# Performance work log

Hardware: AMD Instinct MI355X
Metric: run time of the kernel (lower is better)

The kernel has to match this reference:

```python
import math
import jax, jax.numpy as jnp
import numpy as np

EPS = 1e-5

def lstm(x, Wih, Whh, b):
    # x: [N,T,D]; PyTorch gate order i,f,g,o; b = b_ih + b_hh combined
    N = x.shape[0]
    H = Whh.shape[1]
    gx = jnp.einsum('ntd,gd->ntg', x, Wih) + b  # [N,T,4H]
    def step(carry, g):
        h, c = carry
        z = g + h @ Whh.T
        i, f, gg, o = jnp.split(z, 4, axis=-1)
        c = jax.nn.sigmoid(f) * c + jax.nn.sigmoid(i) * jnp.tanh(gg)
        h = jax.nn.sigmoid(o) * jnp.tanh(c)
        return (h, c), h
    init = (jnp.zeros((N, H), x.dtype), jnp.zeros((N, H), x.dtype))
    (hN, _), ys = jax.lax.scan(step, init, jnp.swapaxes(gx, 0, 1))
    return jnp.swapaxes(ys, 0, 1), hN  # outputs [N,T,H], h_n [N,H]

def bilstm_layer(x, fW, fU, fb, bW, bU, bb):
    of, _ = lstm(x, fW, fU, fb)
    ob, _ = lstm(x[:, ::-1], bW, bU, bb)
    return jnp.concatenate([of, ob[:, ::-1]], axis=-1)

def layernorm(x, g, b):
    m = jnp.mean(x, -1, keepdims=True)
    v = jnp.mean((x - m) ** 2, -1, keepdims=True)
    return (x - m) * jax.lax.rsqrt(v + EPS) * g + b

def encoder_layer(src, Wq, bq, Wk, bk, Wv, bv, Wo, bo, W1, b1, W2, b2, lng, lnb):
    B, S, d = src.shape
    G, NH = 5, 5
    dk = d // NH
    # group channel shuffle (as in source)
    qs = src.reshape(B, S, G, d // G).swapaxes(-1, -2).reshape(B, S, d)
    q = qs @ Wq.T + bq
    k = q @ Wk.T + bk   # NOTE: source applies W_k/W_v to the projected query
    v = q @ Wv.T + bv
    def heads(t):
        return t.reshape(B, S, NH, dk).transpose(0, 2, 1, 3)
    qh, kh, vh = heads(q), heads(k), heads(v)
    attn = jax.nn.softmax(jnp.einsum('bhqd,bhkd->bhqk', qh, kh) / math.sqrt(dk), axis=-1)
    o = jnp.einsum('bhqk,bhkd->bhqd', attn, vh).transpose(0, 2, 1, 3).reshape(B, S, d)
    o = o @ Wo.T + bo
    src = layernorm(src + o, lng, lnb)          # dropout is identity in eval
    ff = jax.nn.relu(src @ W1.T + b1) @ W2.T + b2
    src = layernorm(src + ff, lng, lnb)         # same LayerNorm params reused
    return src, attn

def _forward(x, qWih, qWhh, qb, kWih, kWhh, kb, vWih, vWhh, vb,
             tWq, tbq, tWk, tbk, tWv, tbv, tWo, tbo, tW1, tb1, tW2, tb2, tlng, tlnb,
             l0fWih, l0fWhh, l0fb, l0bWih, l0bWhh, l0bb,
             l1fWih, l1fWhh, l1fb, l1bWih, l1bWhh, l1bb,
             fc1W, fc1b, fc2W, fc2b):
    B, T, F = x.shape
    H = qWhh.shape[1]
    # per-feature LSTMs: shared weights across features -> batch them
    xf = x.transpose(0, 2, 1).reshape(B * F, T, 1)
    _, hq = lstm(xf, qWih, qWhh, qb)   # [B*F,H]
    _, hk = lstm(xf, kWih, kWhh, kb)   # [B*F,H]
    _, hv = lstm(xf, vWih, vWhh, vb)   # [B*F,1]
    Q = hq.reshape(B, F, H)
    K = hk.reshape(B, F, H)
    V = hv.reshape(B, F)
    # b_ij = (q_i . k_j)/sqrt(H) * v_j, softmax over j
    scores = jnp.einsum('bih,bjh->bij', Q, K) / math.sqrt(H) * V[:, None, :]
    Wsm = jax.nn.softmax(scores, axis=-1)          # [B,F,F] rows indexed by i
    attn_output = jnp.einsum('btj,bij->bti', x, Wsm)  # bmm(x, softmax_b_i)
    b = Wsm.transpose(0, 2, 1)                     # stack(b_list, dim=-1)
    src = jnp.concatenate([x, attn_output], axis=-1)  # [B,T,2F]
    attns = []
    for l in range(2):
        src, a = encoder_layer(src, tWq[l], tbq[l], tWk[l], tbk[l], tWv[l], tbv[l],
                               tWo[l], tbo[l], tW1[l], tb1[l], tW2[l], tb2[l],
                               tlng[l], tlnb[l])
        attns.append(a)
    c = jnp.stack(attns)                           # [2,B,5,T,T]
    out = bilstm_layer(src, l0fWih, l0fWhh, l0fb, l0bWih, l0bWhh, l0bb)
    out = bilstm_layer(out, l1fWih, l1fWhh, l1fb, l1bWih, l1bWhh, l1bb)
    out = jax.nn.relu(out[:, -1, :])               # [B,2H]
    out = jax.nn.relu(out @ fc1W.T + fc1b)
    out = out @ fc2W.T + fc2b                      # [B,1]
    return out, b, c

def setup_inputs() -> dict:
    B, T, F, H = 16, 128, 40, 64
    d = 2 * F
    key = jax.random.key(0)
    ks = iter(jax.random.split(key, 64))
    def n(shape, fan):
        return (jax.random.normal(next(ks), shape) / math.sqrt(fan)).astype(jnp.float32)
    inp = {'x': jax.random.normal(next(ks), (B, T, F), dtype=jnp.float32)}
    # per-feature LSTMs
    inp.update(qWih=n((4 * H, 1), 1), qWhh=n((4 * H, H), H), qb=n((4 * H,), H))
    inp.update(kWih=n((4 * H, 1), 1), kWhh=n((4 * H, H), H), kb=n((4 * H,), H))
    inp.update(vWih=n((4, 1), 1), vWhh=n((4, 1), 1), vb=n((4,), 1))
    # transformer (2 layers stacked on leading axis)
    inp.update(tWq=n((2, d, d), d), tbq=n((2, d), d), tWk=n((2, d, d), d), tbk=n((2, d), d),
               tWv=n((2, d, d), d), tbv=n((2, d), d), tWo=n((2, d, d), d), tbo=n((2, d), d),
               tW1=n((2, 4 * d, d), d), tb1=n((2, 4 * d), d), tW2=n((2, d, 4 * d), 4 * d),
               tb2=n((2, d), 4 * d), tlng=jnp.ones((2, d), jnp.float32), tlnb=jnp.zeros((2, d), jnp.float32))
    # main bidirectional 2-layer LSTM
    inp.update(l0fWih=n((4 * H, d), d), l0fWhh=n((4 * H, H), H), l0fb=n((4 * H,), H),
               l0bWih=n((4 * H, d), d), l0bWhh=n((4 * H, H), H), l0bb=n((4 * H,), H),
               l1fWih=n((4 * H, 2 * H), 2 * H), l1fWhh=n((4 * H, H), H), l1fb=n((4 * H,), H),
               l1bWih=n((4 * H, 2 * H), 2 * H), l1bWhh=n((4 * H, H), H), l1bb=n((4 * H,), H))
    inp.update(fc1W=n((H, 2 * H), 2 * H), fc1b=n((H,), 2 * H), fc2W=n((1, H), H), fc2b=n((1,), H))
    return inp

def reference(x, qWih, qWhh, qb, kWih, kWhh, kb, vWih, vWhh, vb,
              tWq, tbq, tWk, tbk, tWv, tbv, tWo, tbo, tW1, tb1, tW2, tb2, tlng, tlnb,
              l0fWih, l0fWhh, l0fb, l0bWih, l0bWhh, l0bb,
              l1fWih, l1fWhh, l1fb, l1bWih, l1bWhh, l1bb,
              fc1W, fc1b, fc2W, fc2b):
    return _forward(x, qWih, qWhh, qb, kWih, kWhh, kb, vWih, vWhh, vb,
                    tWq, tbq, tWk, tbk, tWv, tbv, tWo, tbo, tW1, tb1, tW2, tb2, tlng, tlnb,
                    l0fWih, l0fWhh, l0fb, l0bWih, l0bWhh, l0bb,
                    l1fWih, l1fWhh, l1fb, l1bWih, l1bWhh, l1bb,
                    fc1W, fc1b, fc2W, fc2b)
```

## Files before the change

kernel.cpp:

```cpp
#include <hip/hip_runtime.h>

__device__ __forceinline__ float sigf(float x){ return 1.0f/(1.0f+__expf(-x)); }
__device__ __forceinline__ float tanhfast(float x){ return 1.0f - 2.0f/(__expf(2.0f*x)+1.0f); }

#define Bn 16
#define Tn 128
#define Fn 40
#define Hn 64
#define Dn 80
#define NHn 5
#define DKn 16
#define FFn 320

#define LD4(p,i) (((const float4*)(p))[i])

#define DECL8(v, p) \
  float4 v##0=LD4(p,0), v##1=LD4(p,1), v##2=LD4(p,2), v##3=LD4(p,3), \
         v##4=LD4(p,4), v##5=LD4(p,5), v##6=LD4(p,6), v##7=LD4(p,7);
#define PIN4(P) asm volatile("" : "+v"(P.x), "+v"(P.y), "+v"(P.z), "+v"(P.w));
#define PIN8(v) PIN4(v##0) PIN4(v##1) PIN4(v##2) PIN4(v##3) PIN4(v##4) PIN4(v##5) \
  PIN4(v##6) PIN4(v##7)

#define ACC8(base) \
  { const float4 h0=hb4[(base)+0]; a += h0.x*w0.x + h0.y*w0.y + h0.z*w0.z + h0.w*w0.w; } \
  { const float4 h1=hb4[(base)+1]; a += h1.x*w1.x + h1.y*w1.y + h1.z*w1.z + h1.w*w1.w; } \
  { const float4 h2=hb4[(base)+2]; a += h2.x*w2.x + h2.y*w2.y + h2.z*w2.z + h2.w*w2.w; } \
  { const float4 h3=hb4[(base)+3]; a += h3.x*w3.x + h3.y*w3.y + h3.z*w3.z + h3.w*w3.w; } \
  { const float4 h4=hb4[(base)+4]; a += h4.x*w4.x + h4.y*w4.y + h4.z*w4.z + h4.w*w4.w; } \
  { const float4 h5=hb4[(base)+5]; a += h5.x*w5.x + h5.y*w5.y + h5.z*w5.z + h5.w*w5.w; } \
  { const float4 h6=hb4[(base)+6]; a += h6.x*w6.x + h6.y*w6.y + h6.z*w6.z + h6.w*w6.w; } \
  { const float4 h7=hb4[(base)+7]; a += h7.x*w7.x + h7.y*w7.y + h7.z*w7.z + h7.w*w7.w; }

__global__ __launch_bounds__(512)
void k_feat_lstm5(
    const float* __restrict__ x,
    const float* __restrict__ qWih, const float* __restrict__ qWhh, const float* __restrict__ qb,
    const float* __restrict__ kWih, const float* __restrict__ kWhh, const float* __restrict__ kb,
    const float* __restrict__ vWih, const float* __restrict__ vWhh, const float* __restrict__ vb,
    float* __restrict__ hq, float* __restrict__ hk, float* __restrict__ hv)
{
  const int blk = blockIdx.x;
  const int t = threadIdx.x;
  if (blk >= 1280){
    const int inst = (blk - 1280)*512 + t;
    if (inst < 640){
      const int bi = inst/Fn, f = inst%Fn;
      const float* xp = x + bi*Tn*Fn + f;
      const float wih0=vWih[0], wih1=vWih[1], wih2=vWih[2], wih3=vWih[3];
      const float u0v=vWhh[0], u1v=vWhh[1], u2v=vWhh[2], u3v=vWhh[3];
      const float c0=vb[0], c1=vb[1], c2=vb[2], c3=vb[3];
      float h=0.f, c=0.f;
      #pragma unroll 1
      for (int tt=0;tt<Tn;++tt){
        float xt = xp[tt*Fn];
        float zi = xt*wih0 + h*u0v + c0;
        float zf = xt*wih1 + h*u1v + c1;
        float zg = xt*wih2 + h*u2v + c2;
        float zo = xt*wih3 + h*u3v + c3;
        c = sigf(zf)*c + sigf(zi)*tanhfast(zg);
        h = sigf(zo)*tanhfast(c);
      }
      hv[inst] = h;
    }
    return;
  }
  const bool isk = blk >= 640;
  const int inst = isk ? blk-640 : blk;
  const int bi = inst/Fn, f = inst%Fn;
  const float* Whh = isk ? kWhh : qWhh;
  const float* Wih = isk ? kWih : qWih;
  const float* bia = isk ? kb  : qb;
  float* outp = isk ? hk : hq;

  const int half = t >> 8;
  const int r    = t & 255;

  DECL8(w, Whh + r*Hn + half*32);
  PIN8(w);
  const float wih = Wih[r];
  const float bb  = bia[r];

  __shared__ __align__(16) float hb[Hn];
  __shared__ float pa[512];
  __shared__ float xls[Tn];

  const float* xp = x + bi*Tn*Fn + f;
  if (t < Tn) xls[t] = xp[t*Fn];
  if (t < Hn) hb[t] = 0.f;
  float c = 0.f, h = 0.f;
  __syncthreads();

  const float4* hb4 = (const float4*)hb;
  const int jbase = half*8;
  #pragma unroll 1
  for (int tt=0;tt<Tn;++tt){
    float a = half ? 0.f : (bb + xls[tt]*wih);
    ACC8(jbase)
    pa[t] = a;
    __syncthreads();
    if (t < Hn){
      const float zi = pa[t    ] + pa[t+256];
      const float zf = pa[t+ 64] + pa[t+320];
      const float zg = pa[t+128] + pa[t+384];
      const float zo = pa[t+192] + pa[t+448];
      c = sigf(zf)*c + sigf(zi)*tanhfast(zg);
      h = sigf(zo)*tanhfast(c);
      hb[t] = h;
    }
    __syncthreads();
  }
  if (t < Hn) outp[inst*Hn + t] = h;
}

__global__ __launch_bounds__(64) void k_featattn(
    const float* __restrict__ hq, const float* __restrict__ hk, const float* __restrict__ hv,
    float* __restrict__ Wsm, float* __restrict__ out_b)
{
  const int blk = blockIdx.x;
  const int bi = blk / Fn, i = blk % Fn;
  const int j = threadIdx.x;
  __shared__ float qrow[Hn];
  qrow[j] = hq[blk*Hn + j];
  __syncthreads();
  float s = -1e30f;
  if (j < Fn){
    const float* krow = hk + (bi*Fn + j)*Hn;
    float a = 0.f;
    #pragma unroll
    for (int h2=0; h2<Hn; ++h2) a += qrow[h2]*krow[h2];
    s = a * 0.125f * hv[bi*Fn + j];
  }
  float m = s;
  #pragma unroll
  for (int off=32; off>0; off>>=1) m = fmaxf(m, __shfl_xor(m, off));
  float e = (j < Fn) ? __expf(s - m) : 0.f;
  float tot = e;
  #pragma unroll
  for (int off=32; off>0; off>>=1) tot += __shfl_xor(tot, off);
  float p = e / tot;
  if (j < Fn){
    Wsm[blk*Fn + j] = p;
    out_b[bi*(Fn*Fn) + j*Fn + i] = p;
  }
}

__global__ __launch_bounds__(128) void k_build_src(
    const float* __restrict__ x, const float* __restrict__ Wsm, float* __restrict__ src)
{
  const int blk = blockIdx.x;
  const int bi = blk / Tn;
  const int tid = threadIdx.x;
  __shared__ float xrow[Fn];
  if (tid < Fn) xrow[tid] = x[blk*Fn + tid];
  __syncthreads();
  if (tid < Fn){
    src[blk*Dn + tid] = xrow[tid];
  } else if (tid < Dn){
    const int i = tid - Fn;
    const float* wrow = Wsm + (bi*Fn + i)*Fn;
    float a = 0.f;
    #pragma unroll
    for (int j2=0;j2<Fn;++j2) a += xrow[j2]*wrow[j2];
    src[blk*Dn + tid] = a;
  }
}

__global__ __launch_bounds__(128) void k_qkv(
    const float* __restrict__ src,
    const float* __restrict__ Wq, const float* __restrict__ bq,
    const float* __restrict__ Wk, const float* __restrict__ bk,
    const float* __restrict__ Wv, const float* __restrict__ bv,
    float* __restrict__ q, float* __restrict__ k, float* __restrict__ v)
{
  const int row = blockIdx.x;
  const int t = threadIdx.x;
  __shared__ float qs[Dn];
  __shared__ float qrow[Dn];
  if (t < Dn) qs[t] = src[row*Dn + (t%5)*16 + t/5];
  __syncthreads();
  if (t < Dn){
    const float* wr = Wq + t*Dn;
    float a = bq[t];
    #pragma unroll 8
    for (int d2=0; d2<Dn; ++d2) a += qs[d2]*wr[d2];
    qrow[t] = a;
    q[row*Dn + t] = a;
  }
  __syncthreads();
  if (t < Dn){
    const float* wk = Wk + t*Dn;
    const float* wv = Wv + t*Dn;
    float ak = bk[t], av = bv[t];
    #pragma unroll 8
    for (int d2=0; d2<Dn; ++d2){ float qq = qrow[d2]; ak += qq*wk[d2]; av += qq*wv[d2]; }
    k[row*Dn + t] = ak;
    v[row*Dn + t] = av;
  }
}

__global__ __launch_bounds__(128) void k_attn(
    const float* __restrict__ q, const float* __restrict__ k, const float* __restrict__ v,
    float* __restrict__ o, float* __restrict__ c_out)
{
  const int s1 = blockIdx.x, h = blockIdx.y, bi = blockIdx.z;
  const int s2 = threadIdx.x;
  __shared__ float qf[DKn];
  __shared__ float p[Tn];
  __shared__ float red_m[2];
  __shared__ float red_s[2];
  if (s2 < DKn) qf[s2] = q[(bi*Tn + s1)*Dn + h*DKn + s2];
  __syncthreads();
  const float* krow = k + (bi*Tn + s2)*Dn + h*DKn;
  float a = 0.f;
  #pragma unroll
  for (int d2=0; d2<DKn; ++d2) a += qf[d2]*krow[d2];
  a *= 0.25f;
  const int wv_id = s2 >> 6;
  float m = a;
  #pragma unroll
  for (int off=32; off>0; off>>=1) m = fmaxf(m, __shfl_xor(m, off));
  if ((s2 & 63) == 0) red_m[wv_id] = m;
  __syncthreads();
  m = fmaxf(red_m[0], red_m[1]);
  float e = __expf(a - m);
  float tot = e;
  #pragma unroll
  for (int off=32; off>0; off>>=1) tot += __shfl_xor(tot, off);
  if ((s2 & 63) == 0) red_s[wv_id] = tot;
  __syncthreads();
  tot = red_s[0] + red_s[1];
  float pv = e / tot;
  p[s2] = pv;
  c_out[((bi*NHn + h)*Tn + s1)*Tn + s2] = pv;
  __syncthreads();
  if (s2 < DKn){
    const float* vcol = v + bi*Tn*Dn + h*DKn + s2;
    float acc = 0.f;
    for (int j2=0;j2<Tn;++j2) acc += p[j2]*vcol[j2*Dn];
    o[(bi*Tn + s1)*Dn + h*DKn + s2] = acc;
  }
}

__global__ __launch_bounds__(320) void k_oln_ffln(
    const float* __restrict__ o, const float* __restrict__ Wo, const float* __restrict__ bo,
    const float* __restrict__ W1, const float* __restrict__ b1,
    const float* __restrict__ W2, const float* __restrict__ b2,
    const float* __restrict__ lng, const float* __restrict__ lnb, float* __restrict__ src)
{
  const int row = blockIdx.x;
  const int t = threadIdx.x;
  __shared__ float orow[Dn];
  __shared__ float s1row[Dn];
  __shared__ float h1[FFn];
  __shared__ float red[128];
  if (t < Dn) orow[t] = o[row*Dn + t];
  __syncthreads();
  float val = 0.f;
  if (t < Dn){
    const float* wr = Wo + t*Dn;
    float a = bo[t];
    #pragma unroll 8
    for (int d2=0; d2<Dn; ++d2) a += orow[d2]*wr[d2];
    val = a + src[row*Dn + t];
  }
  if (t < 128) red[t] = (t < Dn) ? val : 0.f;
  __syncthreads();
  for (int s=64; s>0; s>>=1){ if (t < s) red[t] += red[t+s]; __syncthreads(); }
  float mean = red[0] * (1.f/Dn);
  __syncthreads();
  if (t < 128){ float dv = (t < Dn) ? (val - mean) : 0.f; red[t] = dv*dv; }
  __syncthreads();
  for (int s=64; s>0; s>>=1){ if (t < s) red[t] += red[t+s]; __syncthreads(); }
  float rstd = rsqrtf(red[0]*(1.f/Dn) + 1e-5f);
  if (t < Dn) s1row[t] = (val - mean)*rstd*lng[t] + lnb[t];
  __syncthreads();
  {
    const float* wr = W1 + t*Dn;
    float a = b1[t];
    #pragma unroll 8
    for (int d2=0; d2<Dn; ++d2) a += s1row[d2]*wr[d2];
    h1[t] = fmaxf(a, 0.f);
  }
  __syncthreads();
  float val2 = 0.f;
  if (t < Dn){
    const float* wr = W2 + t*FFn;
    float a = b2[t];
    #pragma unroll 8
    for (int d2=0; d2<FFn; ++d2) a += h1[d2]*wr[d2];
    val2 = a + s1row[t];
  }
  if (t < 128) red[t] = (t < Dn) ? val2 : 0.f;
  __syncthreads();
  for (int s=64; s>0; s>>=1){ if (t < s) red[t] += red[t+s]; __syncthreads(); }
  mean = red[0] * (1.f/Dn);
  __syncthreads();
  if (t < 128){ float dv = (t < Dn) ? (val2 - mean) : 0.f; red[t] = dv*dv; }
  __syncthreads();
  for (int s=64; s>0; s>>=1){ if (t < s) red[t] += red[t+s]; __syncthreads(); }
  rstd = rsqrtf(red[0]*(1.f/Dn) + 1e-5f);
  if (t < Dn) src[row*Dn + t] = (val2 - mean)*rstd*lng[t] + lnb[t];
}

__global__ __launch_bounds__(256) void k_gx(
    const float* __restrict__ X, int inD,
    const float* __restrict__ WihF, const float* __restrict__ bF,
    const float* __restrict__ WihB, const float* __restrict__ bB,
    float* __restrict__ gx)
{
  const int row = blockIdx.x;
  const int dir = blockIdx.y;
  const int g = threadIdx.x;
  __shared__ float xs[128];
  for (int d2=g; d2<inD; d2+=256) xs[d2] = X[row*inD + d2];
  __syncthreads();
  const float* W  = dir ? WihB : WihF;
  const float* bb = dir ? bB  : bF;
  const float* wr = W + g*inD;
  float a = bb[g];
  for (int d2=0; d2<inD; ++d2) a += xs[d2]*wr[d2];
  gx[dir*(Bn*Tn*256) + row*256 + g] = a;
}

__global__ __launch_bounds__(512)
void k_bilstm_rec5(
    const float* __restrict__ gx,
    const float* __restrict__ WhhF, const float* __restrict__ WhhB,
    float* __restrict__ outp)
{
  const int n = blockIdx.x;
  const int dir = blockIdx.y;
  const int t = threadIdx.x;
  const int half = t >> 8;
  const int r    = t & 255;
  const float* Whh = dir ? WhhB : WhhF;
  DECL8(w, Whh + r*Hn + half*32);
  PIN8(w);

  __shared__ __align__(16) float hb[Hn];
  __shared__ float pa[512];
  if (t < Hn) hb[t] = 0.f;
  float c = 0.f, h = 0.f;
  __syncthreads();

  const float* gxd = gx + dir*(Bn*Tn*256) + n*Tn*256;
  const float4* hb4 = (const float4*)hb;
  const int jbase = half*8;
  const int t0 = dir ? Tn-1 : 0;
  float g0 = half ? 0.f : gxd[t0*256 + r];
  #pragma unroll 1
  for (int step=0; step<Tn; ++step){
    const int tt = dir ? (Tn-1-step) : step;
    int tn = dir ? (Tn-2-step) : (step+1);
    tn = max(0, min(Tn-1, tn));
    const float p0 = half ? 0.f : gxd[tn*256 + r];
    float a = g0;
    ACC8(jbase)
    pa[t] = a;
    __syncthreads();
    if (t < Hn){
      const float zi = pa[t    ] + pa[t+256];
      const float zf = pa[t+ 64] + pa[t+320];
      const float zg = pa[t+128] + pa[t+384];
      const float zo = pa[t+192] + pa[t+448];
      c = sigf(zf)*c + sigf(zi)*tanhfast(zg);
      h = sigf(zo)*tanhfast(c);
      hb[t] = h;
      outp[(n*Tn + tt)*128 + dir*Hn + t] = h;
    }
    __syncthreads();
    g0 = p0;
  }
}

__global__ __launch_bounds__(128) void k_final(
    const float* __restrict__ out1,
    const float* __restrict__ fc1W, const float* __restrict__ fc1b,
    const float* __restrict__ fc2W, const float* __restrict__ fc2b,
    float* __restrict__ outp)
{
  const int n = blockIdx.x;
  const int t = threadIdx.x;
  __shared__ float r[128];
  __shared__ float a1[64];
  r[t] = fmaxf(out1[(n*Tn + (Tn-1))*128 + t], 0.f);
  __syncthreads();
  if (t < 64){
    const float* wr = fc1W + t*128;
    float a = fc1b[t];
    #pragma unroll 8
    for (int d2=0; d2<128; ++d2) a += r[d2]*wr[d2];
    a1[t] = fmaxf(a, 0.f);
  }
  __syncthreads();
  if (t == 0){
    float a = fc2b[0];
    #pragma unroll 8
    for (int d2=0; d2<64; ++d2) a += a1[d2]*fc2W[d2];
    outp[n] = a;
  }
}

extern "C" void kernel_launch(void* const* d_in, const int* in_sizes, int n_in,
                              void* d_out, int out_size, void* d_ws, size_t ws_size,
                              hipStream_t stream)
{
  const float* x     = (const float*)d_in[0];
  const float* qWih  = (const float*)d_in[1];
  const float* qWhh  = (const float*)d_in[2];
  const float* qb    = (const float*)d_in[3];
  const float* kWih  = (const float*)d_in[4];
  const float* kWhh  = (const float*)d_in[5];
  const float* kb    = (const float*)d_in[6];
  const float* vWih  = (const float*)d_in[7];
  const float* vWhh  = (const float*)d_in[8];
  const float* vb    = (const float*)d_in[9];
  const float* tWq   = (const float*)d_in[10];
  const float* tbq   = (const float*)d_in[11];
  const float* tWk   = (const float*)d_in[12];
  const float* tbk   = (const float*)d_in[13];
  const float* tWv   = (const float*)d_in[14];
  const float* tbv   = (const float*)d_in[15];
  const float* tWo   = (const float*)d_in[16];
  const float* tbo   = (const float*)d_in[17];
  const float* tW1   = (const float*)d_in[18];
  const float* tb1   = (const float*)d_in[19];
  const float* tW2   = (const float*)d_in[20];
  const float* tb2   = (const float*)d_in[21];
  const float* tlng  = (const float*)d_in[22];
  const float* tlnb  = (const float*)d_in[23];
  const float* l0fWih= (const float*)d_in[24];
  const float* l0fWhh= (const float*)d_in[25];
  const float* l0fb  = (const float*)d_in[26];
  const float* l0bWih= (const float*)d_in[27];
  const float* l0bWhh= (const float*)d_in[28];
  const float* l0bb  = (const float*)d_in[29];
  const float* l1fWih= (const float*)d_in[30];
  const float* l1fWhh= (const float*)d_in[31];
  const float* l1fb  = (const float*)d_in[32];
  const float* l1bWih= (const float*)d_in[33];
  const float* l1bWhh= (const float*)d_in[34];
  const float* l1bb  = (const float*)d_in[35];
  const float* fc1W  = (const float*)d_in[36];
  const float* fc1b  = (const float*)d_in[37];
  const float* fc2W  = (const float*)d_in[38];
  const float* fc2b  = (const float*)d_in[39];

  float* ws  = (float*)d_ws;
  float* hq  = ws;
  float* hk  = hq  + 640*64;
  float* hv  = hk  + 640*64;
  float* Wsm = hv  + 640;
  float* src = Wsm + 16*40*40;
  float* q   = src + 16*128*80;
  float* k   = q   + 16*128*80;
  float* v   = k   + 16*128*80;
  float* o   = v   + 16*128*80;
  float* gx  = o   + 16*128*80;
  float* lout0 = gx + 2*16*128*256;
  float* lout1 = lout0 + 16*128*128;

  float* outp  = (float*)d_out;
  float* out_b = outp + 16;
  float* out_c = out_b + 16*40*40;

  k_feat_lstm5<<<1282, 512, 0, stream>>>(x, qWih,qWhh,qb, kWih,kWhh,kb, vWih,vWhh,vb, hq,hk,hv);
  k_featattn<<<640, 64, 0, stream>>>(hq, hk, hv, Wsm, out_b);
  k_build_src<<<2048, 128, 0, stream>>>(x, Wsm, src);
  for (int l=0; l<2; ++l){
    k_qkv<<<2048, 128, 0, stream>>>(src, tWq + l*Dn*Dn, tbq + l*Dn,
                                    tWk + l*Dn*Dn, tbk + l*Dn,
                                    tWv + l*Dn*Dn, tbv + l*Dn, q, k, v);
    k_attn<<<dim3(128,5,16), 128, 0, stream>>>(q, k, v, o, out_c + (size_t)l*16*5*128*128);
    k_oln_ffln<<<2048, 320, 0, stream>>>(o, tWo + l*Dn*Dn, tbo + l*Dn,
                                         tW1 + l*FFn*Dn, tb1 + l*FFn,
                                         tW2 + l*Dn*FFn, tb2 + l*Dn,
                                         tlng + l*Dn, tlnb + l*Dn, src);
  }
  k_gx<<<dim3(2048,2), 256, 0, stream>>>(src, 80, l0fWih, l0fb, l0bWih, l0bb, gx);
  k_bilstm_rec5<<<dim3(16,2), 512, 0, stream>>>(gx, l0fWhh, l0bWhh, lout0);
  k_gx<<<dim3(2048,2), 256, 0, stream>>>(lout0, 128, l1fWih, l1fb, l1bWih, l1bb, gx);
  k_bilstm_rec5<<<dim3(16,2), 512, 0, stream>>>(gx, l1fWhh, l1bWhh, lout1);
  k_final<<<16, 128, 0, stream>>>(lout1, fc1W, fc1b, fc2W, fc2b, outp);
}
```

Measured before the change: 794.4 us.

## Rework feature LSTM thread mapping, split attention PV reduction, tile gx rows

The feature LSTM now uses 128 threads per instance. Each thread holds two full 64-wide Whh rows in pinned registers, so the i/g gates stay in registers and only the f/o gates go through shared memory. The attention PV product is split across all 128 threads with a shared-memory partial reduction, replacing the loop where 16 threads each ran 128 iterations. The gx input projection processes 8 rows per block with float4 weight loads, reusing each weight row across rows. The per-thread register load grows to about 128 pinned floats and the feature LSTM's parallelism per block drops.

```diff
diff --git a/kernel.cpp b/kernel.cpp
--- a/kernel.cpp
+++ b/kernel.cpp
@@ -12,15 +12,24 @@
 #define DKn 16
 #define FFn 320
 
+#define LOAD_PIN_ROW(dst, srcp)                                        \
+  {                                                                    \
+    _Pragma("unroll")                                                  \
+    for (int jj=0; jj<16; ++jj){                                       \
+      float4 tv = *(const float4*)((srcp) + 4*jj);                     \
+      dst[4*jj]=tv.x; dst[4*jj+1]=tv.y; dst[4*jj+2]=tv.z; dst[4*jj+3]=tv.w; \
+    }                                                                  \
+    _Pragma("unroll")                                                  \
+    for (int jj=0; jj<64; ++jj){ asm volatile("" : "+v"(dst[jj])); }   \
+  }
+
 #define LD4(p,i) (((const float4*)(p))[i])
-
 #define DECL8(v, p) \
   float4 v##0=LD4(p,0), v##1=LD4(p,1), v##2=LD4(p,2), v##3=LD4(p,3), \
          v##4=LD4(p,4), v##5=LD4(p,5), v##6=LD4(p,6), v##7=LD4(p,7);
 #define PIN4(P) asm volatile("" : "+v"(P.x), "+v"(P.y), "+v"(P.z), "+v"(P.w));
 #define PIN8(v) PIN4(v##0) PIN4(v##1) PIN4(v##2) PIN4(v##3) PIN4(v##4) PIN4(v##5) \
   PIN4(v##6) PIN4(v##7)
-
 #define ACC8(base) \
   { const float4 h0=hb4[(base)+0]; a += h0.x*w0.x + h0.y*w0.y + h0.z*w0.z + h0.w*w0.w; } \
   { const float4 h1=hb4[(base)+1]; a += h1.x*w1.x + h1.y*w1.y + h1.z*w1.z + h1.w*w1.w; } \
@@ -31,8 +40,7 @@
   { const float4 h6=hb4[(base)+6]; a += h6.x*w6.x + h6.y*w6.y + h6.z*w6.z + h6.w*w6.w; } \
   { const float4 h7=hb4[(base)+7]; a += h7.x*w7.x + h7.y*w7.y + h7.z*w7.z + h7.w*w7.w; }
 
-__global__ __launch_bounds__(512)
-void k_feat_lstm5(
+__global__ __launch_bounds__(128,1) void k_feat_lstm2(
     const float* __restrict__ x,
     const float* __restrict__ qWih, const float* __restrict__ qWhh, const float* __restrict__ qb,
     const float* __restrict__ kWih, const float* __restrict__ kWhh, const float* __restrict__ kb,
@@ -40,28 +48,26 @@
     float* __restrict__ hq, float* __restrict__ hk, float* __restrict__ hv)
 {
   const int blk = blockIdx.x;
-  const int t = threadIdx.x;
+  const int l = threadIdx.x;
   if (blk >= 1280){
-    const int inst = (blk - 1280)*512 + t;
-    if (inst < 640){
-      const int bi = inst/Fn, f = inst%Fn;
-      const float* xp = x + bi*Tn*Fn + f;
-      const float wih0=vWih[0], wih1=vWih[1], wih2=vWih[2], wih3=vWih[3];
-      const float u0v=vWhh[0], u1v=vWhh[1], u2v=vWhh[2], u3v=vWhh[3];
-      const float c0=vb[0], c1=vb[1], c2=vb[2], c3=vb[3];
-      float h=0.f, c=0.f;
-      #pragma unroll 1
-      for (int tt=0;tt<Tn;++tt){
-        float xt = xp[tt*Fn];
-        float zi = xt*wih0 + h*u0v + c0;
-        float zf = xt*wih1 + h*u1v + c1;
-        float zg = xt*wih2 + h*u2v + c2;
-        float zo = xt*wih3 + h*u3v + c3;
-        c = sigf(zf)*c + sigf(zi)*tanhfast(zg);
-        h = sigf(zo)*tanhfast(c);
-      }
-      hv[inst] = h;
+    const int inst = (blk - 1280)*128 + l;
+    const int bi = inst/Fn, f = inst%Fn;
+    const float* xp = x + bi*Tn*Fn + f;
+    const float wih0=vWih[0], wih1=vWih[1], wih2=vWih[2], wih3=vWih[3];
+    const float u0=vWhh[0], u1=vWhh[1], u2=vWhh[2], u3=vWhh[3];
+    const float c0=vb[0], c1=vb[1], c2=vb[2], c3=vb[3];
+    float h=0.f, c=0.f;
+    #pragma unroll 1
+    for (int t=0;t<Tn;++t){
+      float xt = xp[t*Fn];
+      float zi = xt*wih0 + h*u0 + c0;
+      float zf = xt*wih1 + h*u1 + c1;
+      float zg = xt*wih2 + h*u2 + c2;
+      float zo = xt*wih3 + h*u3 + c3;
+      c = sigf(zf)*c + sigf(zi)*tanhfast(zg);
+      h = sigf(zo)*tanhfast(c);
     }
+    hv[inst] = h;
     return;
   }
   const bool isk = blk >= 640;
@@ -72,44 +78,49 @@
   const float* bia = isk ? kb  : qb;
   float* outp = isk ? hk : hq;
 
-  const int half = t >> 8;
-  const int r    = t & 255;
-
-  DECL8(w, Whh + r*Hn + half*32);
-  PIN8(w);
-  const float wih = Wih[r];
-  const float bb  = bia[r];
+  const int r0 = l;
+  const int r1 = l + 128;
+
+  float w0[Hn], w1[Hn];
+  LOAD_PIN_ROW(w0, Whh + r0*Hn);
+  LOAD_PIN_ROW(w1, Whh + r1*Hn);
+  const float wih0 = Wih[r0], wih1 = Wih[r1];
+  const float bb0 = bia[r0], bb1 = bia[r1];
 
   __shared__ __align__(16) float hb[Hn];
-  __shared__ float pa[512];
+  __shared__ float zb[4*Hn];
   __shared__ float xls[Tn];
 
   const float* xp = x + bi*Tn*Fn + f;
-  if (t < Tn) xls[t] = xp[t*Fn];
-  if (t < Hn) hb[t] = 0.f;
+  xls[l] = xp[l*Fn];
+  if (l < Hn) hb[l] = 0.f;
   float c = 0.f, h = 0.f;
   __syncthreads();
 
   const float4* hb4 = (const float4*)hb;
-  const int jbase = half*8;
   #pragma unroll 1
-  for (int tt=0;tt<Tn;++tt){
-    float a = half ? 0.f : (bb + xls[tt]*wih);
-    ACC8(jbase)
-    pa[t] = a;
+  for (int t=0;t<Tn;++t){
+    const float xt = xls[t];
+    float a0 = bb0 + xt*wih0;
+    float a1 = bb1 + xt*wih1;
+    #pragma unroll
+    for (int jj=0; jj<16; ++jj){
+      const float4 hv4 = hb4[jj];
+      a0 += hv4.x*w0[4*jj  ] + hv4.y*w0[4*jj+1] + hv4.z*w0[4*jj+2] + hv4.w*w0[4*jj+3];
+      a1 += hv4.x*w1[4*jj  ] + hv4.y*w1[4*jj+1] + hv4.z*w1[4*jj+2] + hv4.w*w1[4*jj+3];
+    }
+    if (l >= Hn){ zb[l] = a0; zb[l+128] = a1; }
     __syncthreads();
-    if (t < Hn){
-      const float zi = pa[t    ] + pa[t+256];
-      const float zf = pa[t+ 64] + pa[t+320];
-      const float zg = pa[t+128] + pa[t+384];
-      const float zo = pa[t+192] + pa[t+448];
+    if (l < Hn){
+      const float zi = a0, zg = a1;
+      const float zf = zb[l+64], zo = zb[l+192];
       c = sigf(zf)*c + sigf(zi)*tanhfast(zg);
       h = sigf(zo)*tanhfast(c);
-      hb[t] = h;
+      hb[l] = h;
     }
     __syncthreads();
   }
-  if (t < Hn) outp[inst*Hn + t] = h;
+  if (l < Hn) outp[inst*Hn + l] = h;
 }
 
 __global__ __launch_bounds__(64) void k_featattn(
@@ -206,6 +217,7 @@
   const int s2 = threadIdx.x;
   __shared__ float qf[DKn];
   __shared__ float p[Tn];
+  __shared__ float pa[128];
   __shared__ float red_m[2];
   __shared__ float red_s[2];
   if (s2 < DKn) qf[s2] = q[(bi*Tn + s1)*Dn + h*DKn + s2];
@@ -233,10 +245,23 @@
   p[s2] = pv;
   c_out[((bi*NHn + h)*Tn + s1)*Tn + s2] = pv;
   __syncthreads();
+  {
+    const int d    = s2 & 15;
+    const int part = s2 >> 4;
+    const float* vcol = v + bi*Tn*Dn + h*DKn + d;
+    float acc = 0.f;
+    #pragma unroll
+    for (int jj=0; jj<16; ++jj){
+      const int j2 = part*16 + jj;
+      acc += p[j2]*vcol[j2*Dn];
+    }
+    pa[s2] = acc;
+  }
+  __syncthreads();
   if (s2 < DKn){
-    const float* vcol = v + bi*Tn*Dn + h*DKn + s2;
     float acc = 0.f;
-    for (int j2=0;j2<Tn;++j2) acc += p[j2]*vcol[j2*Dn];
+    #pragma unroll
+    for (int k2=0; k2<8; ++k2) acc += pa[k2*16 + s2];
     o[(bi*Tn + s1)*Dn + h*DKn + s2] = acc;
   }
 }
@@ -302,24 +327,39 @@
   if (t < Dn) src[row*Dn + t] = (val2 - mean)*rstd*lng[t] + lnb[t];
 }
 
-__global__ __launch_bounds__(256) void k_gx(
-    const float* __restrict__ X, int inD,
+template<int IND>
+__global__ __launch_bounds__(256) void k_gx8(
+    const float* __restrict__ X,
     const float* __restrict__ WihF, const float* __restrict__ bF,
     const float* __restrict__ WihB, const float* __restrict__ bB,
     float* __restrict__ gx)
 {
-  const int row = blockIdx.x;
+  const int row0 = blockIdx.x * 8;
   const int dir = blockIdx.y;
   const int g = threadIdx.x;
-  __shared__ float xs[128];
-  for (int d2=g; d2<inD; d2+=256) xs[d2] = X[row*inD + d2];
+  __shared__ float xs[8][IND];
+  #pragma unroll
+  for (int rr=0; rr<8; ++rr)
+    for (int d2=g; d2<IND; d2+=256) xs[rr][d2] = X[(row0+rr)*IND + d2];
   __syncthreads();
   const float* W  = dir ? WihB : WihF;
   const float* bb = dir ? bB  : bF;
-  const float* wr = W + g*inD;
-  float a = bb[g];
-  for (int d2=0; d2<inD; ++d2) a += xs[d2]*wr[d2];
-  gx[dir*(Bn*Tn*256) + row*256 + g] = a;
+  const float* wr = W + g*IND;
+  float acc[8];
+  const float b0 = bb[g];
+  #pragma unroll
+  for (int rr=0; rr<8; ++rr) acc[rr] = b0;
+  #pragma unroll 4
+  for (int d2=0; d2<IND; d2+=4){
+    const float4 wv = *(const float4*)(wr + d2);
+    #pragma unroll
+    for (int rr=0; rr<8; ++rr){
+      acc[rr] += xs[rr][d2]*wv.x + xs[rr][d2+1]*wv.y + xs[rr][d2+2]*wv.z + xs[rr][d2+3]*wv.w;
+    }
+  }
+  float* gxd = gx + dir*(Bn*Tn*256);
+  #pragma unroll
+  for (int rr=0; rr<8; ++rr) gxd[(row0+rr)*256 + g] = acc[rr];
 }
 
 __global__ __launch_bounds__(512)
@@ -464,7 +504,7 @@
   float* out_b = outp + 16;
   float* out_c = out_b + 16*40*40;
 
-  k_feat_lstm5<<<1282, 512, 0, stream>>>(x, qWih,qWhh,qb, kWih,kWhh,kb, vWih,vWhh,vb, hq,hk,hv);
+  k_feat_lstm2<<<1285, 128, 0, stream>>>(x, qWih,qWhh,qb, kWih,kWhh,kb, vWih,vWhh,vb, hq,hk,hv);
   k_featattn<<<640, 64, 0, stream>>>(hq, hk, hv, Wsm, out_b);
   k_build_src<<<2048, 128, 0, stream>>>(x, Wsm, src);
   for (int l=0; l<2; ++l){
@@ -477,9 +517,9 @@
                                          tW2 + l*Dn*FFn, tb2 + l*Dn,
                                          tlng + l*Dn, tlnb + l*Dn, src);
   }
-  k_gx<<<dim3(2048,2), 256, 0, stream>>>(src, 80, l0fWih, l0fb, l0bWih, l0bb, gx);
+  k_gx8<80><<<dim3(256,2), 256, 0, stream>>>(src, l0fWih, l0fb, l0bWih, l0bb, gx);
   k_bilstm_rec5<<<dim3(16,2), 512, 0, stream>>>(gx, l0fWhh, l0bWhh, lout0);
-  k_gx<<<dim3(2048,2), 256, 0, stream>>>(lout0, 128, l1fWih, l1fb, l1bWih, l1bb, gx);
+  k_gx8<128><<<dim3(256,2), 256, 0, stream>>>(lout0, l1fWih, l1fb, l1bWih, l1bb, gx);
   k_bilstm_rec5<<<dim3(16,2), 512, 0, stream>>>(gx, l1fWhh, l1bWhh, lout1);
   k_final<<<16, 128, 0, stream>>>(lout1, fc1W, fc1b, fc2W, fc2b, outp);
 }
```

New measurement: 663.1 us. 1.2x faster.
